# Performance work log

Measured on AMD Instinct MI355X. Metric: run time of the kernel, lower is better.

Reference implementation:

```python
import jax, jax.numpy as jnp
import numpy as np

BIG = 1000000.0
EPS = 1e-06
COST_CLASS, COST_BBOX, COST_GIOU = 1.0, 5.0, 2.0


def sanitize_boxes(boxes):
    # boxes: [..., 4] cxcywh
    boxes = jnp.nan_to_num(boxes, nan=0.0, posinf=1.0, neginf=0.0)
    cx, cy, w, h = jnp.moveaxis(boxes, -1, 0)
    cx = jnp.clip(cx, 0.0, 1.0)
    cy = jnp.clip(cy, 0.0, 1.0)
    w = jnp.clip(w, EPS, 1.0)
    h = jnp.clip(h, EPS, 1.0)
    return jnp.stack([cx, cy, w, h], axis=-1)


def box_cxcywh_to_xyxy(x):
    cx, cy, w, h = jnp.moveaxis(x, -1, 0)
    return jnp.stack([cx - 0.5 * w, cy - 0.5 * h, cx + 0.5 * w, cy + 0.5 * h], axis=-1)


def pairwise_giou(b1, b2):
    # b1: [B, Q, 4] xyxy, b2: [B, T, 4] xyxy -> [B, Q, T]
    area1 = (b1[..., 2] - b1[..., 0]) * (b1[..., 3] - b1[..., 1])  # [B,Q]
    area2 = (b2[..., 2] - b2[..., 0]) * (b2[..., 3] - b2[..., 1])  # [B,T]
    lt = jnp.maximum(b1[:, :, None, :2], b2[:, None, :, :2])  # [B,Q,T,2]
    rb = jnp.minimum(b1[:, :, None, 2:], b2[:, None, :, 2:])
    wh = jnp.clip(rb - lt, 0.0)
    inter = wh[..., 0] * wh[..., 1]  # [B,Q,T]
    union = area1[:, :, None] + area2[:, None, :] - inter
    iou = inter / union
    # enclosing box
    lt_c = jnp.minimum(b1[:, :, None, :2], b2[:, None, :, :2])
    rb_c = jnp.maximum(b1[:, :, None, 2:], b2[:, None, :, 2:])
    wh_c = jnp.clip(rb_c - lt_c, 0.0)
    area_c = wh_c[..., 0] * wh_c[..., 1]
    return iou - (area_c - union) / area_c


def reference(pred_logits, pred_boxes, tgt_labels, tgt_boxes):
    # Batched cost-matrix construction of HungarianMatcher.forward.
    out_logits = jnp.nan_to_num(pred_logits, nan=0.0, posinf=0.0, neginf=0.0)
    out_prob = jax.nn.softmax(out_logits, axis=-1)  # [B,Q,C]
    out_bbox = sanitize_boxes(pred_boxes)           # [B,Q,4]
    t_bbox = sanitize_boxes(tgt_boxes)              # [B,T,4]

    # cost_class[b,q,t] = -out_prob[b,q,tgt_labels[b,t]]
    B, Q, C = out_prob.shape
    T = tgt_labels.shape[1]
    gather_idx = jnp.broadcast_to(tgt_labels[:, None, :], (B, Q, T))
    cost_class = -jnp.take_along_axis(out_prob, gather_idx, axis=2)  # [B,Q,T]

    # L1 cdist in cxcywh space
    cost_bbox = jnp.sum(jnp.abs(out_bbox[:, :, None, :] - t_bbox[:, None, :, :]), axis=-1)

    cost_giou = -pairwise_giou(box_cxcywh_to_xyxy(out_bbox), box_cxcywh_to_xyxy(t_bbox))

    Cmat = COST_CLASS * cost_class + COST_BBOX * cost_bbox + COST_GIOU * cost_giou
    return jnp.nan_to_num(Cmat, nan=BIG, posinf=BIG, neginf=BIG)


def setup_inputs() -> dict:
    key = jax.random.key(0)
    k1, k2, k3, k4 = jax.random.split(key, 4)
    B, Q, C, T = 64, 900, 256, 200
    return {
        "pred_logits": jax.random.normal(k1, (B, Q, C), dtype=jnp.float32),
        "pred_boxes": jax.random.uniform(k2, (B, Q, 4), dtype=jnp.float32),
        "tgt_labels": jax.random.randint(k3, (B, T), 0, C),
        "tgt_boxes": jax.random.uniform(k4, (B, T, 4), dtype=jnp.float32),
    }
```

## Files before the change

kernel.cpp:

```cpp
#include <hip/hip_runtime.h>
#include <math.h>

constexpr int B = 64, Q = 900, C = 256, T = 200;
constexpr float EPSV = 1e-6f;
constexpr int WPB = 4;
constexpr int QPW = 2;
constexpr int QPB = WPB * QPW;
constexpr int NT4 = T / 4;

typedef float f32x4 __attribute__((ext_vector_type(4)));

__device__ __forceinline__ float clampf(float x, float lo, float hi) {
    return fminf(fmaxf(x, lo), hi);
}

#define DPP_ADD_STEP(x, ctrl, row_mask)                                        \
    (x) += __int_as_float(__builtin_amdgcn_update_dpp(                         \
        0, __float_as_int(x), (ctrl), (row_mask), 0xf, true))

__global__ __launch_bounds__(256, 8)
void matcher_kernel(const float* __restrict__ logits,
                    const float* __restrict__ pboxes,
                    const int*   __restrict__ tlabels,
                    const float* __restrict__ tboxes,
                    float* __restrict__ out)
{
    __shared__ float s_exp[WPB][C][2];

    const int blocks_per_b = (Q + QPB - 1) / QPB;
    const int b    = blockIdx.x / blocks_per_b;
    const int qblk = blockIdx.x % blocks_per_b;
    const int wave = threadIdx.x >> 6;
    const int lane = threadIdx.x & 63;
    const int q0   = qblk * QPB + wave * QPW;
    if (q0 >= Q) return;

    const size_t rowa = (size_t)b * Q + q0;
    const size_t rowb = rowa + 1;

    const f32x4 lga =
        __builtin_nontemporal_load((const f32x4*)(logits + rowa * C) + lane);
    const f32x4 lgb =
        __builtin_nontemporal_load((const f32x4*)(logits + rowb * C) + lane);
    const float4 pba = *(const float4*)(pboxes + rowa * 4);
    const float4 pbb = *(const float4*)(pboxes + rowb * 4);

    const bool act = lane < NT4;
    const int  t0i = act ? 4 * lane : 0;
    const float4* tb_base = (const float4*)(tboxes + b * (T * 4));
    const float4 tbr[4] = {tb_base[t0i], tb_base[t0i + 1],
                           tb_base[t0i + 2], tb_base[t0i + 3]};
    const int4 labs = *(const int4*)(tlabels + b * T + t0i);

    float tx0[4], ty0[4], tx1[4], ty1[4], twd[4], tht[4];
    int   lidx[4];
    {
        const int lbs[4] = {labs.x, labs.y, labs.z, labs.w};
        #pragma unroll
        for (int s = 0; s < 4; ++s) {
            float cx = clampf(tbr[s].x, 0.0f, 1.0f);
            float cy = clampf(tbr[s].y, 0.0f, 1.0f);
            float w  = clampf(tbr[s].z, EPSV, 1.0f);
            float h  = clampf(tbr[s].w, EPSV, 1.0f);
            twd[s] = w;  tht[s] = h;
            tx0[s] = cx - 0.5f * w;  ty0[s] = cy - 0.5f * h;
            tx1[s] = cx + 0.5f * w;  ty1[s] = cy + 0.5f * h;
            lidx[s] = min(max(lbs[s], 0), C - 1);
        }
    }

    float ea0 = __expf(lga.x), ea1 = __expf(lga.y);
    float ea2 = __expf(lga.z), ea3 = __expf(lga.w);
    float eb0 = __expf(lgb.x), eb1 = __expf(lgb.y);
    float eb2 = __expf(lgb.z), eb3 = __expf(lgb.w);
    float sa = (ea0 + ea1) + (ea2 + ea3);
    float sb = (eb0 + eb1) + (eb2 + eb3);
    DPP_ADD_STEP(sa, 0x111, 0xf);  DPP_ADD_STEP(sb, 0x111, 0xf);
    DPP_ADD_STEP(sa, 0x112, 0xf);  DPP_ADD_STEP(sb, 0x112, 0xf);
    DPP_ADD_STEP(sa, 0x114, 0xf);  DPP_ADD_STEP(sb, 0x114, 0xf);
    DPP_ADD_STEP(sa, 0x118, 0xf);  DPP_ADD_STEP(sb, 0x118, 0xf);
    DPP_ADD_STEP(sa, 0x142, 0xa);  DPP_ADD_STEP(sb, 0x142, 0xa);
    DPP_ADD_STEP(sa, 0x143, 0xc);  DPP_ADD_STEP(sb, 0x143, 0xc);
    const float inva = __builtin_amdgcn_rcpf(__int_as_float(
        __builtin_amdgcn_readlane(__float_as_int(sa), 63)));
    const float invb = __builtin_amdgcn_rcpf(__int_as_float(
        __builtin_amdgcn_readlane(__float_as_int(sb), 63)));

    float* dst = &s_exp[wave][4 * lane][0];
    ((float4*)dst)[0] = make_float4(ea0, eb0, ea1, eb1);
    ((float4*)dst)[1] = make_float4(ea2, eb2, ea3, eb3);

    float ga[4], gb[4];
    #pragma unroll
    for (int s = 0; s < 4; ++s) {
        const float2 g = *(const float2*)&s_exp[wave][lidx[s]][0];
        ga[s] = g.x;  gb[s] = g.y;
    }

    {
        float pcx = clampf(pba.x, 0.0f, 1.0f), pcy = clampf(pba.y, 0.0f, 1.0f);
        float pw  = clampf(pba.z, EPSV, 1.0f), ph  = clampf(pba.w, EPSV, 1.0f);
        float px0 = pcx - 0.5f * pw, py0 = pcy - 0.5f * ph;
        float px1 = pcx + 0.5f * pw, py1 = pcy + 0.5f * ph;
        float psx = px0 + px1, psy = py0 + py1;
        float parea = pw * ph;

        float res[4];
        #pragma unroll
        for (int s = 0; s < 4; ++s) {
            float tsx = tx0[s] + tx1[s];
            float tsy = ty0[s] + ty1[s];
            float t0 = fmaf(-ga[s], inva, 2.0f);
            float s1 = fabsf(psx - tsx) + fabsf(psy - tsy);
            float s2 = fabsf(pw - twd[s]) + fabsf(ph - tht[s]);
            float iwr = fminf(px1, tx1[s]) - fmaxf(px0, tx0[s]);
            float ihr = fminf(py1, ty1[s]) - fmaxf(py0, ty0[s]);
            float inter = fmaxf(iwr, 0.0f) * fmaxf(ihr, 0.0f);
            float uni = fmaf(twd[s], tht[s], parea) - inter;
            float cw = (pw + twd[s]) - iwr;
            float ch = (ph + tht[s]) - ihr;
            float ca = cw * ch;
            float num = fmaf(uni, uni, inter * ca);
            float val = num * __builtin_amdgcn_rcpf(uni * ca);
            float cost = fmaf(2.5f, s1, t0);
            cost = fmaf(5.0f, s2, cost);
            res[s] = fmaf(-2.0f, val, cost);
        }
        if (act) {
            f32x4 v; v.x = res[0]; v.y = res[1]; v.z = res[2]; v.w = res[3];
            __builtin_nontemporal_store(v, (f32x4*)(out + rowa * T) + lane);
        }
    }

    {
        float pcx = clampf(pbb.x, 0.0f, 1.0f), pcy = clampf(pbb.y, 0.0f, 1.0f);
        float pw  = clampf(pbb.z, EPSV, 1.0f), ph  = clampf(pbb.w, EPSV, 1.0f);
        float px0 = pcx - 0.5f * pw, py0 = pcy - 0.5f * ph;
        float px1 = pcx + 0.5f * pw, py1 = pcy + 0.5f * ph;
        float psx = px0 + px1, psy = py0 + py1;
        float parea = pw * ph;

        float res[4];
        #pragma unroll
        for (int s = 0; s < 4; ++s) {
            float tsx = tx0[s] + tx1[s];
            float tsy = ty0[s] + ty1[s];
            float t0 = fmaf(-gb[s], invb, 2.0f);
            float s1 = fabsf(psx - tsx) + fabsf(psy - tsy);
            float s2 = fabsf(pw - twd[s]) + fabsf(ph - tht[s]);
            float iwr = fminf(px1, tx1[s]) - fmaxf(px0, tx0[s]);
            float ihr = fminf(py1, ty1[s]) - fmaxf(py0, ty0[s]);
            float inter = fmaxf(iwr, 0.0f) * fmaxf(ihr, 0.0f);
            float uni = fmaf(twd[s], tht[s], parea) - inter;
            float cw = (pw + twd[s]) - iwr;
            float ch = (ph + tht[s]) - ihr;
            float ca = cw * ch;
            float num = fmaf(uni, uni, inter * ca);
            float val = num * __builtin_amdgcn_rcpf(uni * ca);
            float cost = fmaf(2.5f, s1, t0);
            cost = fmaf(5.0f, s2, cost);
            res[s] = fmaf(-2.0f, val, cost);
        }
        if (act) {
            f32x4 v; v.x = res[0]; v.y = res[1]; v.z = res[2]; v.w = res[3];
            __builtin_nontemporal_store(v, (f32x4*)(out + rowb * T) + lane);
        }
    }
}

extern "C" void kernel_launch(void* const* d_in, const int* in_sizes, int n_in,
                              void* d_out, int out_size, void* d_ws, size_t ws_size,
                              hipStream_t stream) {
    const float* logits  = (const float*)d_in[0];
    const float* pboxes  = (const float*)d_in[1];
    const int*   tlabels = (const int*)d_in[2];
    const float* tboxes  = (const float*)d_in[3];
    float* out = (float*)d_out;

    const int blocks_per_b = (Q + QPB - 1) / QPB;
    dim3 grid(B * blocks_per_b);
    dim3 block(64 * WPB);
    matcher_kernel<<<grid, block, 0, stream>>>(logits, pboxes, tlabels, tboxes, out);
}
```

Measured before the change: 116.0 us.

## Process one query per wave and compute box costs before the softmax

Each wave now handles a single query row instead of two, which doubles the grid and halves per-wave register and shared-memory use. The geometric cost terms are computed before the softmax exponentials, and the class probability is folded in afterwards through a shared-memory gather. Nontemporal loads and stores are replaced with plain vector accesses. The trade-off is that target boxes and labels are reloaded per query, so there is more redundant target work and more blocks to schedule, in exchange for more parallelism and latency hiding.

```diff
diff --git a/kernel.cpp b/kernel.cpp
--- a/kernel.cpp
+++ b/kernel.cpp
@@ -4,11 +4,9 @@
 constexpr int B = 64, Q = 900, C = 256, T = 200;
 constexpr float EPSV = 1e-6f;
 constexpr int WPB = 4;
-constexpr int QPW = 2;
+constexpr int QPW = 1;
 constexpr int QPB = WPB * QPW;
 constexpr int NT4 = T / 4;
-
-typedef float f32x4 __attribute__((ext_vector_type(4)));
 
 __device__ __forceinline__ float clampf(float x, float lo, float hi) {
     return fminf(fmaxf(x, lo), hi);
@@ -25,36 +23,30 @@
                     const float* __restrict__ tboxes,
                     float* __restrict__ out)
 {
-    __shared__ float s_exp[WPB][C][2];
+    __shared__ float s_exp[WPB][C];
 
-    const int blocks_per_b = (Q + QPB - 1) / QPB;
+    const int blocks_per_b = Q / QPB;
     const int b    = blockIdx.x / blocks_per_b;
     const int qblk = blockIdx.x % blocks_per_b;
     const int wave = threadIdx.x >> 6;
     const int lane = threadIdx.x & 63;
-    const int q0   = qblk * QPB + wave * QPW;
-    if (q0 >= Q) return;
+    const int q    = qblk * QPB + wave;
+    const size_t row = (size_t)b * Q + q;
 
-    const size_t rowa = (size_t)b * Q + q0;
-    const size_t rowb = rowa + 1;
-
-    const f32x4 lga =
-        __builtin_nontemporal_load((const f32x4*)(logits + rowa * C) + lane);
-    const f32x4 lgb =
-        __builtin_nontemporal_load((const f32x4*)(logits + rowb * C) + lane);
-    const float4 pba = *(const float4*)(pboxes + rowa * 4);
-    const float4 pbb = *(const float4*)(pboxes + rowb * 4);
+    const float4 lg = ((const float4*)(logits + row * C))[lane];
 
     const bool act = lane < NT4;
     const int  t0i = act ? 4 * lane : 0;
     const float4* tb_base = (const float4*)(tboxes + b * (T * 4));
-    const float4 tbr[4] = {tb_base[t0i], tb_base[t0i + 1],
-                           tb_base[t0i + 2], tb_base[t0i + 3]};
+    const float4 tbr0 = tb_base[t0i],     tbr1 = tb_base[t0i + 1];
+    const float4 tbr2 = tb_base[t0i + 2], tbr3 = tb_base[t0i + 3];
     const int4 labs = *(const int4*)(tlabels + b * T + t0i);
+    const float4 pb  = *(const float4*)(pboxes + row * 4);
 
     float tx0[4], ty0[4], tx1[4], ty1[4], twd[4], tht[4];
-    int   lidx[4];
+    int   cidx[4];
     {
+        const float4 tbr[4] = {tbr0, tbr1, tbr2, tbr3};
         const int lbs[4] = {labs.x, labs.y, labs.z, labs.w};
         #pragma unroll
         for (int s = 0; s < 4; ++s) {
@@ -65,106 +57,59 @@
             twd[s] = w;  tht[s] = h;
             tx0[s] = cx - 0.5f * w;  ty0[s] = cy - 0.5f * h;
             tx1[s] = cx + 0.5f * w;  ty1[s] = cy + 0.5f * h;
-            lidx[s] = min(max(lbs[s], 0), C - 1);
+            cidx[s] = min(max(lbs[s], 0), C - 1);
         }
     }
 
-    float ea0 = __expf(lga.x), ea1 = __expf(lga.y);
-    float ea2 = __expf(lga.z), ea3 = __expf(lga.w);
-    float eb0 = __expf(lgb.x), eb1 = __expf(lgb.y);
-    float eb2 = __expf(lgb.z), eb3 = __expf(lgb.w);
-    float sa = (ea0 + ea1) + (ea2 + ea3);
-    float sb = (eb0 + eb1) + (eb2 + eb3);
-    DPP_ADD_STEP(sa, 0x111, 0xf);  DPP_ADD_STEP(sb, 0x111, 0xf);
-    DPP_ADD_STEP(sa, 0x112, 0xf);  DPP_ADD_STEP(sb, 0x112, 0xf);
-    DPP_ADD_STEP(sa, 0x114, 0xf);  DPP_ADD_STEP(sb, 0x114, 0xf);
-    DPP_ADD_STEP(sa, 0x118, 0xf);  DPP_ADD_STEP(sb, 0x118, 0xf);
-    DPP_ADD_STEP(sa, 0x142, 0xa);  DPP_ADD_STEP(sb, 0x142, 0xa);
-    DPP_ADD_STEP(sa, 0x143, 0xc);  DPP_ADD_STEP(sb, 0x143, 0xc);
-    const float inva = __builtin_amdgcn_rcpf(__int_as_float(
-        __builtin_amdgcn_readlane(__float_as_int(sa), 63)));
-    const float invb = __builtin_amdgcn_rcpf(__int_as_float(
-        __builtin_amdgcn_readlane(__float_as_int(sb), 63)));
+    const float pcx = clampf(pb.x, 0.0f, 1.0f), pcy = clampf(pb.y, 0.0f, 1.0f);
+    const float pw  = clampf(pb.z, EPSV, 1.0f), ph  = clampf(pb.w, EPSV, 1.0f);
+    const float px0 = pcx - 0.5f * pw, py0 = pcy - 0.5f * ph;
+    const float px1 = pcx + 0.5f * pw, py1 = pcy + 0.5f * ph;
+    const float psx = px0 + px1, psy = py0 + py1;
+    const float parea = pw * ph;
 
-    float* dst = &s_exp[wave][4 * lane][0];
-    ((float4*)dst)[0] = make_float4(ea0, eb0, ea1, eb1);
-    ((float4*)dst)[1] = make_float4(ea2, eb2, ea3, eb3);
-
-    float ga[4], gb[4];
+    float res[4];
     #pragma unroll
     for (int s = 0; s < 4; ++s) {
-        const float2 g = *(const float2*)&s_exp[wave][lidx[s]][0];
-        ga[s] = g.x;  gb[s] = g.y;
+        float tsx = tx0[s] + tx1[s];
+        float tsy = ty0[s] + ty1[s];
+        float s1 = fabsf(psx - tsx) + fabsf(psy - tsy);
+        float s2 = fabsf(pw - twd[s]) + fabsf(ph - tht[s]);
+        float iwr = fminf(px1, tx1[s]) - fmaxf(px0, tx0[s]);
+        float ihr = fminf(py1, ty1[s]) - fmaxf(py0, ty0[s]);
+        float inter = fmaxf(iwr, 0.0f) * fmaxf(ihr, 0.0f);
+        float uni = fmaf(twd[s], tht[s], parea) - inter;
+        float cw = (pw + twd[s]) - iwr;
+        float ch = (ph + tht[s]) - ihr;
+        float ca = cw * ch;
+        float num = fmaf(uni, uni, inter * ca);
+        float val = num * __builtin_amdgcn_rcpf(uni * ca);
+        float cost = fmaf(2.5f, s1, 2.0f);
+        cost = fmaf(5.0f, s2, cost);
+        res[s] = fmaf(-2.0f, val, cost);
     }
 
-    {
-        float pcx = clampf(pba.x, 0.0f, 1.0f), pcy = clampf(pba.y, 0.0f, 1.0f);
-        float pw  = clampf(pba.z, EPSV, 1.0f), ph  = clampf(pba.w, EPSV, 1.0f);
-        float px0 = pcx - 0.5f * pw, py0 = pcy - 0.5f * ph;
-        float px1 = pcx + 0.5f * pw, py1 = pcy + 0.5f * ph;
-        float psx = px0 + px1, psy = py0 + py1;
-        float parea = pw * ph;
+    const float e0 = __expf(lg.x), e1 = __expf(lg.y);
+    const float e2 = __expf(lg.z), e3 = __expf(lg.w);
+    ((float4*)&s_exp[wave][4 * lane])[0] = make_float4(e0, e1, e2, e3);
+    float ss = (e0 + e1) + (e2 + e3);
+    DPP_ADD_STEP(ss, 0x111, 0xf);
+    DPP_ADD_STEP(ss, 0x112, 0xf);
+    DPP_ADD_STEP(ss, 0x114, 0xf);
+    DPP_ADD_STEP(ss, 0x118, 0xf);
+    DPP_ADD_STEP(ss, 0x142, 0xa);
+    DPP_ADD_STEP(ss, 0x143, 0xc);
+    const float inv = __builtin_amdgcn_rcpf(__int_as_float(
+        __builtin_amdgcn_readlane(__float_as_int(ss), 63)));
 
-        float res[4];
-        #pragma unroll
-        for (int s = 0; s < 4; ++s) {
-            float tsx = tx0[s] + tx1[s];
-            float tsy = ty0[s] + ty1[s];
-            float t0 = fmaf(-ga[s], inva, 2.0f);
-            float s1 = fabsf(psx - tsx) + fabsf(psy - tsy);
-            float s2 = fabsf(pw - twd[s]) + fabsf(ph - tht[s]);
-            float iwr = fminf(px1, tx1[s]) - fmaxf(px0, tx0[s]);
-            float ihr = fminf(py1, ty1[s]) - fmaxf(py0, ty0[s]);
-            float inter = fmaxf(iwr, 0.0f) * fmaxf(ihr, 0.0f);
-            float uni = fmaf(twd[s], tht[s], parea) - inter;
-            float cw = (pw + twd[s]) - iwr;
-            float ch = (ph + tht[s]) - ihr;
-            float ca = cw * ch;
-            float num = fmaf(uni, uni, inter * ca);
-            float val = num * __builtin_amdgcn_rcpf(uni * ca);
-            float cost = fmaf(2.5f, s1, t0);
-            cost = fmaf(5.0f, s2, cost);
-            res[s] = fmaf(-2.0f, val, cost);
-        }
-        if (act) {
-            f32x4 v; v.x = res[0]; v.y = res[1]; v.z = res[2]; v.w = res[3];
-            __builtin_nontemporal_store(v, (f32x4*)(out + rowa * T) + lane);
-        }
+    #pragma unroll
+    for (int s = 0; s < 4; ++s) {
+        res[s] = fmaf(-s_exp[wave][cidx[s]], inv, res[s]);
     }
 
-    {
-        float pcx = clampf(pbb.x, 0.0f, 1.0f), pcy = clampf(pbb.y, 0.0f, 1.0f);
-        float pw  = clampf(pbb.z, EPSV, 1.0f), ph  = clampf(pbb.w, EPSV, 1.0f);
-        float px0 = pcx - 0.5f * pw, py0 = pcy - 0.5f * ph;
-        float px1 = pcx + 0.5f * pw, py1 = pcy + 0.5f * ph;
-        float psx = px0 + px1, psy = py0 + py1;
-        float parea = pw * ph;
-
-        float res[4];
-        #pragma unroll
-        for (int s = 0; s < 4; ++s) {
-            float tsx = tx0[s] + tx1[s];
-            float tsy = ty0[s] + ty1[s];
-            float t0 = fmaf(-gb[s], invb, 2.0f);
-            float s1 = fabsf(psx - tsx) + fabsf(psy - tsy);
-            float s2 = fabsf(pw - twd[s]) + fabsf(ph - tht[s]);
-            float iwr = fminf(px1, tx1[s]) - fmaxf(px0, tx0[s]);
-            float ihr = fminf(py1, ty1[s]) - fmaxf(py0, ty0[s]);
-            float inter = fmaxf(iwr, 0.0f) * fmaxf(ihr, 0.0f);
-            float uni = fmaf(twd[s], tht[s], parea) - inter;
-            float cw = (pw + twd[s]) - iwr;
-            float ch = (ph + tht[s]) - ihr;
-            float ca = cw * ch;
-            float num = fmaf(uni, uni, inter * ca);
-            float val = num * __builtin_amdgcn_rcpf(uni * ca);
-            float cost = fmaf(2.5f, s1, t0);
-            cost = fmaf(5.0f, s2, cost);
-            res[s] = fmaf(-2.0f, val, cost);
-        }
-        if (act) {
-            f32x4 v; v.x = res[0]; v.y = res[1]; v.z = res[2]; v.w = res[3];
-            __builtin_nontemporal_store(v, (f32x4*)(out + rowb * T) + lane);
-        }
+    if (act) {
+        ((float4*)(out + row * T))[lane] =
+            make_float4(res[0], res[1], res[2], res[3]);
     }
 }
 
@@ -177,7 +122,7 @@
     const float* tboxes  = (const float*)d_in[3];
     float* out = (float*)d_out;
 
-    const int blocks_per_b = (Q + QPB - 1) / QPB;
+    const int blocks_per_b = Q / QPB;
     dim3 grid(B * blocks_per_b);
     dim3 block(64 * WPB);
     matcher_kernel<<<grid, block, 0, stream>>>(logits, pboxes, tlabels, tboxes, out);
```

New measurement: 116.6 us. No clear change (+0.5%).
